# Kernel tuning notes

Hardware: AMD Instinct MI355X
Metric: run time of the kernel (lower is better)

Reference implementation:

```python
import jax, jax.numpy as jnp
import numpy as np

DY, DO, DI = 16, 256, 256
BS = 4096
EPS = 1e-6


def setup_inputs() -> dict:
    key = jax.random.key(0)
    k1, k2, k3, k4, k5 = jax.random.split(key, 5)
    k = 1.0 / float(np.sqrt(DY * DI))
    return {
        "x": jax.random.normal(k1, (DY * DI, BS), dtype=jnp.float32),
        "rms_params": jnp.ones((DY * DI,), dtype=jnp.float32)
        + 0.01 * jax.random.normal(k2, (DY * DI,), dtype=jnp.float32),
        "w_upper": jax.random.uniform(k3, (DY, DO, DI), minval=-k, maxval=k, dtype=jnp.float32),
        "w_lower": jax.random.uniform(k4, (DY, DO, DI), minval=-k, maxval=k, dtype=jnp.float32),
        "bias": jax.random.uniform(k5, (DY * DO,), minval=-k, maxval=k, dtype=jnp.float32),
    }


def reference(x, rms_params, w_upper, w_lower, bias):
    # x: (dy*di, bs) features-first layout, matching the torch op.
    dy, do, di = w_upper.shape
    bs = x.shape[1]
    # Per-column RMS factor (fc in the original op is shape (bs,)).
    fc = jax.lax.rsqrt(jnp.mean(x * x, axis=0) + EPS)  # (bs,)
    xn = x * rms_params[:, None] * fc[None, :]          # fused norm+scale
    xb = xn.reshape(dy, di, bs)
    # Dyadic structured matmul: upper acts on block d, lower on its paired
    # (reversed) block dy-1-d.
    up = jnp.einsum("doi,dib->dob", w_upper, xb)
    lo = jnp.einsum("doi,dib->dob", w_lower, xb[::-1])
    y = jax.nn.relu(up + lo + bias.reshape(dy, do, 1))
    return y.reshape(dy * do, bs)
```

## Files before the change

kernel.cpp:

```cpp
#include <hip/hip_runtime.h>

#define DYN 16
#define DON 256
#define DIN 256
#define BSN 4096
#define NF 4096
#define KTOT 512

typedef unsigned short u16;
typedef __attribute__((ext_vector_type(8))) short bf16x8;
typedef __attribute__((ext_vector_type(4))) float f32x4;
typedef __attribute__((ext_vector_type(4))) unsigned short u16x4;

static __device__ __forceinline__ u16 f2bf(float f) {
  unsigned u = __builtin_bit_cast(unsigned, f);
  u += 0x7fffu + ((u >> 16) & 1u);
  return (u16)(u >> 16);
}
static __device__ __forceinline__ float bf2f(u16 h) {
  unsigned u = ((unsigned)h) << 16;
  return __builtin_bit_cast(float, u);
}

__global__ __launch_bounds__(256) void k_pre(
    const float* __restrict__ x, const float* __restrict__ wu,
    const float* __restrict__ wl, const float* __restrict__ rms,
    u16* __restrict__ aprep, u16* __restrict__ xbf,
    float* __restrict__ partial) {
  __shared__ u16 tile[128 * 132];
  const int t = threadIdx.x;
  if (blockIdx.x < 1024) {
    int e = blockIdx.x * 256 + t;
    int row = e >> 6;
    int k0 = (e & 63) << 3;
    int d = row >> 8;
    const float* src;
    const float* rp;
    if (k0 < 256) {
      src = wu + (size_t)row * 256 + k0;
      rp  = rms + d * 256 + k0;
    } else {
      src = wl + (size_t)row * 256 + (k0 - 256);
      rp  = rms + (DYN - 1 - d) * 256 + (k0 - 256);
    }
    float4 s0 = *reinterpret_cast<const float4*>(src);
    float4 s1 = *reinterpret_cast<const float4*>(src + 4);
    float4 r0 = *reinterpret_cast<const float4*>(rp);
    float4 r1 = *reinterpret_cast<const float4*>(rp + 4);
    bf16x8 o;
    o[0] = (short)f2bf(s0.x * r0.x); o[1] = (short)f2bf(s0.y * r0.y);
    o[2] = (short)f2bf(s0.z * r0.z); o[3] = (short)f2bf(s0.w * r0.w);
    o[4] = (short)f2bf(s1.x * r1.x); o[5] = (short)f2bf(s1.y * r1.y);
    o[6] = (short)f2bf(s1.z * r1.z); o[7] = (short)f2bf(s1.w * r1.w);
    *reinterpret_cast<bf16x8*>(aprep + (size_t)row * KTOT + k0) = o;
    return;
  }
  const int bid = blockIdx.x - 1024;
  const int bt = bid & 31, ft = bid >> 5;
  const float* xb = x + (size_t)ft * 128 * BSN + bt * 128;
  const int frow = t >> 5, b4 = (t & 31) * 4;
  #pragma unroll
  for (int p = 0; p < 16; ++p) {
    int f = p * 8 + frow;
    float4 v = *reinterpret_cast<const float4*>(xb + (size_t)f * BSN + b4);
    u16x4 h;
    h[0] = f2bf(v.x); h[1] = f2bf(v.y); h[2] = f2bf(v.z); h[3] = f2bf(v.w);
    *reinterpret_cast<u16x4*>(&tile[f * 132 + b4]) = h;
  }
  __syncthreads();
  const int chunk = t & 15;
  const int bg = t >> 4;
  #pragma unroll
  for (int p = 0; p < 8; ++p) {
    int b = bg + p * 16;
    float s = 0.f;
    bf16x8 w;
    #pragma unroll
    for (int jj = 0; jj < 8; ++jj) {
      int j = (jj + chunk) & 7;
      u16 v = tile[(chunk * 8 + j) * 132 + b];
      float xv = bf2f(v);
      s += xv * xv;
      w[j] = (short)v;
    }
    *reinterpret_cast<bf16x8*>(
        xbf + (size_t)(bt * 128 + b) * NF + ft * 128 + chunk * 8) = w;
    #pragma unroll
    for (int m = 1; m < 16; m <<= 1) s += __shfl_xor(s, m, 64);
    if (chunk == 0) partial[ft * BSN + bt * 128 + b] = s;
  }
}

__global__ __launch_bounds__(512, 2) void k_gemm(
    const u16* __restrict__ aprep, const u16* __restrict__ xbf,
    const float* __restrict__ partial, const float* __restrict__ bias,
    float* __restrict__ out) {
  extern __shared__ char smem[];
  float* fcl = (float*)(smem + 73728);
  const int bid = blockIdx.x;
  const int dp = bid & 7;
  const int d = ((bid >> 3) & 1) ? (15 - dp) : dp;
  const int bt = bid >> 4;
  const int b0 = bt * 256;
  const int t = threadIdx.x;
  const int wave = t >> 6, lane = t & 63;
  const int lhi = lane >> 4, llo = lane & 15;
  const int wm = wave >> 2, wn = wave & 3;
  const int kmask = ((llo >> 1) & 7) << 4;

  auto stage = [&](int slot, int kt, int frL) {
    const int fbase = (kt < 8) ? (d * 256 + kt * 32)
                               : ((15 - d) * 256 + (kt - 8) * 32);
    #pragma unroll
    for (int j = 0; j < 2; ++j) {
      int c = j * 512 + t;
      int cl = c ^ ((c >> 3) & 7);
      int r = cl >> 2, kc = cl & 3;
      const u16* g = xbf + (size_t)(b0 + r) * NF + fbase + kc * 8;
      unsigned lbase = (unsigned)(slot * 24576 + (j * 512 + wave * 64) * 16);
      __builtin_amdgcn_global_load_lds(
          (const __attribute__((address_space(1))) unsigned int*)g,
          (__attribute__((address_space(3))) unsigned int*)(smem + lbase),
          16, 0, 0);
    }
    {
      int c = t;
      int cl = c ^ ((c >> 3) & 7);
      int r = cl >> 2, kc = cl & 3;
      const u16* g = aprep + (size_t)(frL + r) * KTOT + kt * 32 + kc * 8;
      unsigned lbase = (unsigned)(slot * 24576 + 16384 + (wave * 64) * 16);
      __builtin_amdgcn_global_load_lds(
          (const __attribute__((address_space(1))) unsigned int*)g,
          (__attribute__((address_space(3))) unsigned int*)(smem + lbase),
          16, 0, 0);
    }
  };

  if (t < 256) {
    float fs = 0.f;
    #pragma unroll
    for (int i = 0; i < 32; ++i) fs += partial[i * BSN + b0 + t];
    fcl[t] = rsqrtf(fs * (1.0f / 4096.0f) + 1e-6f);
  }

  f32x4 acc[8][2];
  float4 e1[16];

  #pragma unroll
  for (int L = 0; L < 2; ++L) {
    const int frL = d * 256 + L * 128;
    #pragma unroll
    for (int m = 0; m < 8; ++m)
      #pragma unroll
      for (int n = 0; n < 2; ++n)
        acc[m][n] = f32x4{0.f, 0.f, 0.f, 0.f};

    stage(0, 0, frL);
    stage(1, 1, frL);
    asm volatile("s_waitcnt vmcnt(3)\n\ts_barrier" ::: "memory");

    #pragma unroll
    for (int kt = 0; kt < 16; ++kt) {
      const int slot = kt % 3;
      const char* sA = (const char*)smem + slot * 24576;
      const char* sB = sA + 16384;
      if (L == 1) {
        int m = kt >> 1, n = kt & 1;
        size_t ob = (size_t)(d * 256 + wn * 32 + n * 16 + llo) * BSN +
                    b0 + wm * 128 + m * 16 + lhi * 4;
        *reinterpret_cast<float4*>(out + ob) = e1[kt];
      }
      if (kt < 14) stage((kt + 2) % 3, kt + 2, frL);

      bf16x8 af[8], bq[2];
      #pragma unroll
      for (int m = 0; m < 8; ++m) {
        int row = wm * 128 + m * 16 + llo;
        af[m] = *reinterpret_cast<const bf16x8*>(
            sA + ((row * 64 + lhi * 16) ^ kmask));
      }
      #pragma unroll
      for (int n = 0; n < 2; ++n) {
        int row = wn * 32 + n * 16 + llo;
        bq[n] = *reinterpret_cast<const bf16x8*>(
            sB + ((row * 64 + lhi * 16) ^ kmask));
      }
      __builtin_amdgcn_s_setprio(1);
      #pragma unroll
      for (int m = 0; m < 8; ++m)
        #pragma unroll
        for (int n = 0; n < 2; ++n)
          acc[m][n] = __builtin_amdgcn_mfma_f32_16x16x32_bf16(
              af[m], bq[n], acc[m][n], 0, 0, 0);
      __builtin_amdgcn_s_setprio(0);

      if (kt < 14) {
        if (L == 1) {
          asm volatile("s_waitcnt vmcnt(4)\n\ts_barrier" ::: "memory");
        } else {
          asm volatile("s_waitcnt vmcnt(3)\n\ts_barrier" ::: "memory");
        }
      } else if (kt == 14) {
        if (L == 1) {
          asm volatile("s_waitcnt vmcnt(1)\n\ts_barrier" ::: "memory");
        } else {
          asm volatile("s_waitcnt vmcnt(0)\n\ts_barrier" ::: "memory");
        }
      }
    }

    #pragma unroll
    for (int m = 0; m < 8; ++m) {
      int lb = wm * 128 + m * 16 + lhi * 4;
      float4 fq = *reinterpret_cast<const float4*>(&fcl[lb]);
      #pragma unroll
      for (int n = 0; n < 2; ++n) {
        int fo = frL + wn * 32 + n * 16 + llo;
        float bv = bias[fo];
        float4 v;
        v.x = fmaxf(acc[m][n][0] * fq.x + bv, 0.f);
        v.y = fmaxf(acc[m][n][1] * fq.y + bv, 0.f);
        v.z = fmaxf(acc[m][n][2] * fq.z + bv, 0.f);
        v.w = fmaxf(acc[m][n][3] * fq.w + bv, 0.f);
        if (L == 0) {
          e1[m * 2 + n] = v;
        } else {
          *reinterpret_cast<float4*>(
              out + (size_t)fo * BSN + b0 + lb) = v;
        }
      }
    }
    if (L == 0) __builtin_amdgcn_s_barrier();
  }
}

extern "C" void kernel_launch(void* const* d_in, const int* in_sizes, int n_in,
                              void* d_out, int out_size, void* d_ws, size_t ws_size,
                              hipStream_t stream) {
  (void)in_sizes; (void)n_in; (void)out_size; (void)ws_size;
  const float* x    = (const float*)d_in[0];
  const float* rms  = (const float*)d_in[1];
  const float* wu   = (const float*)d_in[2];
  const float* wl   = (const float*)d_in[3];
  const float* bias = (const float*)d_in[4];
  float* out = (float*)d_out;

  char* ws = (char*)d_ws;
  u16* xbf      = (u16*)ws;
  u16* aprep    = (u16*)(ws + 33554432);
  float* partial = (float*)(ws + 37748736);

  k_pre<<<2048, 256, 0, stream>>>(x, wu, wl, rms, aprep, xbf, partial);
  k_gemm<<<256, 512, 74752, stream>>>(aprep, xbf, partial, bias, out);
}
```

Before: 58.67 us.

## Split GEMM blocks over output-feature halves and stage A fragments in halves

Each k_gemm block previously computed two 128-row output halves one after the other, holding the first half's results in registers and storing them during the second pass. Now the grid doubles to 512 blocks, each block handles one output half, the L loop and its deferred-store buffer are removed, and the A-fragment loads are split into two groups of four to reduce register pressure. Launch bounds are raised to 4 blocks per SM so occupancy can go up. The cost is that every x tile in LDS is loaded twice, once per half, and fcl is recomputed per block. With 74752 bytes of LDS per block, the 4-blocks-per-SM hint may not actually be reachable.

Result: faster. 57.51 us (-2.0%).

```diff
diff --git a/kernel.cpp b/kernel.cpp
--- a/kernel.cpp
+++ b/kernel.cpp
@@ -91,7 +91,7 @@
   }
 }
 
-__global__ __launch_bounds__(512, 2) void k_gemm(
+__global__ __launch_bounds__(512, 4) void k_gemm(
     const u16* __restrict__ aprep, const u16* __restrict__ xbf,
     const float* __restrict__ partial, const float* __restrict__ bias,
     float* __restrict__ out) {
@@ -99,16 +99,19 @@
   float* fcl = (float*)(smem + 73728);
   const int bid = blockIdx.x;
   const int dp = bid & 7;
-  const int d = ((bid >> 3) & 1) ? (15 - dp) : dp;
-  const int bt = bid >> 4;
+  const int s = bid >> 3;
+  const int d = (s & 1) ? (15 - dp) : dp;
+  const int fh = (s >> 1) & 1;
+  const int bt = s >> 2;
   const int b0 = bt * 256;
+  const int fr0 = d * 256 + fh * 128;
   const int t = threadIdx.x;
   const int wave = t >> 6, lane = t & 63;
   const int lhi = lane >> 4, llo = lane & 15;
   const int wm = wave >> 2, wn = wave & 3;
   const int kmask = ((llo >> 1) & 7) << 4;
 
-  auto stage = [&](int slot, int kt, int frL) {
+  auto stage = [&](int slot, int kt) {
     const int fbase = (kt < 8) ? (d * 256 + kt * 32)
                                : ((15 - d) * 256 + (kt - 8) * 32);
     #pragma unroll
@@ -127,7 +130,7 @@
       int c = t;
       int cl = c ^ ((c >> 3) & 7);
       int r = cl >> 2, kc = cl & 3;
-      const u16* g = aprep + (size_t)(frL + r) * KTOT + kt * 32 + kc * 8;
+      const u16* g = aprep + (size_t)(fr0 + r) * KTOT + kt * 32 + kc * 8;
       unsigned lbase = (unsigned)(slot * 24576 + 16384 + (wave * 64) * 16);
       __builtin_amdgcn_global_load_lds(
           (const __attribute__((address_space(1))) unsigned int*)g,
@@ -144,93 +147,80 @@
   }
 
   f32x4 acc[8][2];
-  float4 e1[16];
-
-  #pragma unroll
-  for (int L = 0; L < 2; ++L) {
-    const int frL = d * 256 + L * 128;
-    #pragma unroll
-    for (int m = 0; m < 8; ++m)
+  #pragma unroll
+  for (int m = 0; m < 8; ++m)
+    #pragma unroll
+    for (int n = 0; n < 2; ++n)
+      acc[m][n] = f32x4{0.f, 0.f, 0.f, 0.f};
+
+  stage(0, 0);
+  stage(1, 1);
+  asm volatile("s_waitcnt vmcnt(3)\n\ts_barrier" ::: "memory");
+
+  for (int kt = 0; kt < 16; ++kt) {
+    const int slot = kt % 3;
+    const char* sA = (const char*)smem + slot * 24576;
+    const char* sB = sA + 16384;
+    if (kt < 14) stage((kt + 2) % 3, kt + 2);
+
+    bf16x8 bq[2], af[4];
+    #pragma unroll
+    for (int n = 0; n < 2; ++n) {
+      int row = wn * 32 + n * 16 + llo;
+      bq[n] = *reinterpret_cast<const bf16x8*>(
+          sB + ((row * 64 + lhi * 16) ^ kmask));
+    }
+    #pragma unroll
+    for (int m = 0; m < 4; ++m) {
+      int row = wm * 128 + m * 16 + llo;
+      af[m] = *reinterpret_cast<const bf16x8*>(
+          sA + ((row * 64 + lhi * 16) ^ kmask));
+    }
+    __builtin_amdgcn_s_setprio(1);
+    #pragma unroll
+    for (int m = 0; m < 4; ++m)
       #pragma unroll
       for (int n = 0; n < 2; ++n)
-        acc[m][n] = f32x4{0.f, 0.f, 0.f, 0.f};
-
-    stage(0, 0, frL);
-    stage(1, 1, frL);
-    asm volatile("s_waitcnt vmcnt(3)\n\ts_barrier" ::: "memory");
-
-    #pragma unroll
-    for (int kt = 0; kt < 16; ++kt) {
-      const int slot = kt % 3;
-      const char* sA = (const char*)smem + slot * 24576;
-      const char* sB = sA + 16384;
-      if (L == 1) {
-        int m = kt >> 1, n = kt & 1;
-        size_t ob = (size_t)(d * 256 + wn * 32 + n * 16 + llo) * BSN +
-                    b0 + wm * 128 + m * 16 + lhi * 4;
-        *reinterpret_cast<float4*>(out + ob) = e1[kt];
-      }
-      if (kt < 14) stage((kt + 2) % 3, kt + 2, frL);
-
-      bf16x8 af[8], bq[2];
+        acc[m][n] = __builtin_amdgcn_mfma_f32_16x16x32_bf16(
+            af[m], bq[n], acc[m][n], 0, 0, 0);
+    __builtin_amdgcn_s_setprio(0);
+    #pragma unroll
+    for (int m = 0; m < 4; ++m) {
+      int row = wm * 128 + 64 + m * 16 + llo;
+      af[m] = *reinterpret_cast<const bf16x8*>(
+          sA + ((row * 64 + lhi * 16) ^ kmask));
+    }
+    __builtin_amdgcn_s_setprio(1);
+    #pragma unroll
+    for (int m = 0; m < 4; ++m)
       #pragma unroll
-      for (int m = 0; m < 8; ++m) {
-        int row = wm * 128 + m * 16 + llo;
-        af[m] = *reinterpret_cast<const bf16x8*>(
-            sA + ((row * 64 + lhi * 16) ^ kmask));
-      }
-      #pragma unroll
-      for (int n = 0; n < 2; ++n) {
-        int row = wn * 32 + n * 16 + llo;
-        bq[n] = *reinterpret_cast<const bf16x8*>(
-            sB + ((row * 64 + lhi * 16) ^ kmask));
-      }
-      __builtin_amdgcn_s_setprio(1);
-      #pragma unroll
-      for (int m = 0; m < 8; ++m)
-        #pragma unroll
-        for (int n = 0; n < 2; ++n)
-          acc[m][n] = __builtin_amdgcn_mfma_f32_16x16x32_bf16(
-              af[m], bq[n], acc[m][n], 0, 0, 0);
-      __builtin_amdgcn_s_setprio(0);
-
-      if (kt < 14) {
-        if (L == 1) {
-          asm volatile("s_waitcnt vmcnt(4)\n\ts_barrier" ::: "memory");
-        } else {
-          asm volatile("s_waitcnt vmcnt(3)\n\ts_barrier" ::: "memory");
-        }
-      } else if (kt == 14) {
-        if (L == 1) {
-          asm volatile("s_waitcnt vmcnt(1)\n\ts_barrier" ::: "memory");
-        } else {
-          asm volatile("s_waitcnt vmcnt(0)\n\ts_barrier" ::: "memory");
-        }
-      }
-    }
-
-    #pragma unroll
-    for (int m = 0; m < 8; ++m) {
-      int lb = wm * 128 + m * 16 + lhi * 4;
-      float4 fq = *reinterpret_cast<const float4*>(&fcl[lb]);
-      #pragma unroll
-      for (int n = 0; n < 2; ++n) {
-        int fo = frL + wn * 32 + n * 16 + llo;
-        float bv = bias[fo];
-        float4 v;
-        v.x = fmaxf(acc[m][n][0] * fq.x + bv, 0.f);
-        v.y = fmaxf(acc[m][n][1] * fq.y + bv, 0.f);
-        v.z = fmaxf(acc[m][n][2] * fq.z + bv, 0.f);
-        v.w = fmaxf(acc[m][n][3] * fq.w + bv, 0.f);
-        if (L == 0) {
-          e1[m * 2 + n] = v;
-        } else {
-          *reinterpret_cast<float4*>(
-              out + (size_t)fo * BSN + b0 + lb) = v;
-        }
-      }
-    }
-    if (L == 0) __builtin_amdgcn_s_barrier();
+      for (int n = 0; n < 2; ++n)
+        acc[4 + m][n] = __builtin_amdgcn_mfma_f32_16x16x32_bf16(
+            af[m], bq[n], acc[4 + m][n], 0, 0, 0);
+    __builtin_amdgcn_s_setprio(0);
+
+    if (kt < 14) {
+      asm volatile("s_waitcnt vmcnt(3)\n\ts_barrier" ::: "memory");
+    } else if (kt == 14) {
+      asm volatile("s_waitcnt vmcnt(0)\n\ts_barrier" ::: "memory");
+    }
+  }
+
+  #pragma unroll
+  for (int m = 0; m < 8; ++m) {
+    int lb = wm * 128 + m * 16 + lhi * 4;
+    float4 fq = *reinterpret_cast<const float4*>(&fcl[lb]);
+    #pragma unroll
+    for (int n = 0; n < 2; ++n) {
+      int fo = fr0 + wn * 32 + n * 16 + llo;
+      float bv = bias[fo];
+      float4 v;
+      v.x = fmaxf(acc[m][n][0] * fq.x + bv, 0.f);
+      v.y = fmaxf(acc[m][n][1] * fq.y + bv, 0.f);
+      v.z = fmaxf(acc[m][n][2] * fq.z + bv, 0.f);
+      v.w = fmaxf(acc[m][n][3] * fq.w + bv, 0.f);
+      *reinterpret_cast<float4*>(out + (size_t)fo * BSN + b0 + lb) = v;
+    }
   }
 }
 
@@ -251,5 +241,5 @@
   float* partial = (float*)(ws + 37748736);
 
   k_pre<<<2048, 256, 0, stream>>>(x, wu, wl, rms, aprep, xbf, partial);
-  k_gemm<<<256, 512, 74752, stream>>>(aprep, xbf, partial, bias, out);
-}
+  k_gemm<<<512, 512, 74752, stream>>>(aprep, xbf, partial, bias, out);
+}
```
